# Performance work log

Measured on AMD Instinct MI355X. Metric: run time of the kernel, lower is better.

Reference implementation:

```python
import jax, jax.numpy as jnp
import numpy as np

B = 1024       # repertoires (batch)
TCR = 100      # instances (TCRs) per repertoire
FEAT = 15      # feature_num (conv in_channels)
AA = 24        # aa_num (sequence length)
KS = [2, 3, 4, 5, 6, 7]
FN = [3, 3, 3, 2, 2, 1]
NINP = 14      # sum(FN)
EPS = 1e-5     # BatchNorm eps


def sparsemax(z):
    # z: (B, K); sparsemax along axis 1 (Martins & Astudillo 2016)
    K = z.shape[1]
    zs = -jnp.sort(-z, axis=1)               # descending sort
    cs = jnp.cumsum(zs, axis=1)
    k = jnp.arange(1, K + 1, dtype=z.dtype)
    support = 1.0 + k * zs > cs              # (B, K) bool
    ksel = jnp.sum(support, axis=1, keepdims=True).astype(jnp.int32)  # support size
    tau = (jnp.take_along_axis(cs, ksel - 1, axis=1) - 1.0) / ksel.astype(z.dtype)
    return jnp.maximum(z - tau, 0.0)


def setup_inputs() -> dict:
    key = jax.random.key(0)
    ks = jax.random.split(key, 12)
    inp = {"x": jax.random.normal(ks[0], (B, TCR, FEAT, AA), dtype=jnp.float32)}
    for i, (h, f) in enumerate(zip(KS, FN)):
        inp[f"cw{i}"] = jax.random.normal(ks[1 + i], (f, FEAT, h), dtype=jnp.float32) * 0.1
        inp[f"cb{i}"] = jnp.zeros((f,), dtype=jnp.float32)
    inp["fc1_w"] = jax.random.normal(ks[7], (NINP, NINP), dtype=jnp.float32) * 0.2
    inp["fc1_b"] = jnp.zeros((NINP,), dtype=jnp.float32)
    inp["waout_w"] = jax.random.normal(ks[8], (1, NINP), dtype=jnp.float32) * 0.2
    inp["decf_w"] = jax.random.normal(ks[9], (NINP, NINP), dtype=jnp.float32) * 0.2
    inp["decf_b"] = jnp.zeros((NINP,), dtype=jnp.float32)
    inp["bn_g"] = jnp.ones((NINP,), dtype=jnp.float32)
    inp["bn_b"] = jnp.zeros((NINP,), dtype=jnp.float32)
    inp["decs_w"] = jax.random.normal(ks[10], (2, NINP), dtype=jnp.float32) * 0.2
    inp["decs_b"] = jnp.zeros((2,), dtype=jnp.float32)
    return inp


def reference(x, cw0, cb0, cw1, cb1, cw2, cb2, cw3, cb3, cw4, cb4, cw5, cb5,
              fc1_w, fc1_b, waout_w, decf_w, decf_b, bn_g, bn_b, decs_w, decs_b):
    xf = x.reshape(-1, FEAT, AA)  # (B*TCR, 15, 24)
    feats = []
    for w, b in ((cw0, cb0), (cw1, cb1), (cw2, cb2), (cw3, cb3), (cw4, cb4), (cw5, cb5)):
        y = jax.lax.conv_general_dilated(xf, w, (1,), 'VALID',
                                         dimension_numbers=('NCH', 'OIH', 'NCH'))
        y = jax.nn.relu(y + b[None, :, None])
        feats.append(jnp.max(y, axis=-1))  # AdaptiveMaxPool1d(1): global max over length
    out = jnp.concatenate(feats, axis=1).reshape(-1, TCR, NINP)  # (B, TCR, 14)
    # fclayer1 + dropout(eval=identity) + relu; applied per-instance so the
    # torch (TCR, B, .) transpose is equivalent to working in (B, TCR, .)
    h = jax.nn.relu(out @ fc1_w.T + fc1_b)                       # (B, TCR, 14)
    attw = sparsemax(h @ waout_w[0])                             # (B, TCR)
    pooled = jnp.einsum('bt,btd->bd', attw, h)                   # bmm(attw[:,None,:], h)
    z = pooled @ decf_w.T + decf_b                               # decoder_f
    mu = jnp.mean(z, axis=0)                                     # BatchNorm1d (batch stats)
    var = jnp.var(z, axis=0)
    z = jax.nn.relu((z - mu) / jnp.sqrt(var + EPS) * bn_g + bn_b)
    logits = z @ decs_w.T + decs_b                               # decoder_s -> (B, 2)
    return logits, attw
```

## Files before the change

kernel.cpp:

```cpp
#include <hip/hip_runtime.h>

typedef unsigned int  u32;
typedef unsigned short u16;

__device__ __forceinline__ float bf2f(u16 u){
    return __uint_as_float(((u32)u) << 16);
}
__device__ __forceinline__ float lo16(u32 v){ return __uint_as_float(v << 16); }
__device__ __forceinline__ float hi16(u32 v){ return __uint_as_float(v & 0xffff0000u); }
__device__ __forceinline__ u16 f2bf(float f){
    u32 x = __float_as_uint(f);
    x += 0x7fffu + ((x >> 16) & 1u);
    return (u16)(x >> 16);
}
__device__ __forceinline__ float ldany(const void* p, int i, bool bf){
    return bf ? bf2f(((const u16*)p)[i]) : ((const float*)p)[i];
}

#define B_      1024
#define TCR_    100
#define NINST   (B_*TCR_)

#define OFF_WL     0
#define OFF_CB     840
#define OFF_FC1W   854
#define OFF_FC1B   1050
#define OFF_WA     1064
#define OFF_DECFW  1078
#define OFF_DECFB  1274
#define OFF_BNG    1288
#define OFF_BNB    1302
#define OFF_DECSW  1316
#define OFF_DECSB  1344

__global__ __launch_bounds__(256) void k_pack(
    const void* cw0, const void* cb0, const void* cw1, const void* cb1,
    const void* cw2, const void* cb2, const void* cw3, const void* cb3,
    const void* cw4, const void* cb4, const void* cw5, const void* cb5,
    const void* fc1_w, const void* fc1_b, const void* waout,
    const void* decf_w, const void* decf_b,
    const void* bn_g, const void* bn_b,
    const void* decs_w, const void* decs_b,
    float* __restrict__ wsP)
{
    const int tid = threadIdx.x;
    const bool bf = (((const u16*)bn_g)[0] == 0x3F80u);

    for (int widx = tid; widx < 840; widx += 256){
        float val;
        if (widx < 90)      { int e = widx;       int c=e/6,  rr=e-c*6,  ff=rr/2, j=rr-ff*2; val=ldany(cw0,(ff*15+c)*2+j,bf); }
        else if (widx < 225){ int e = widx - 90;  int c=e/9,  rr=e-c*9,  ff=rr/3, j=rr-ff*3; val=ldany(cw1,(ff*15+c)*3+j,bf); }
        else if (widx < 405){ int e = widx - 225; int c=e/12, rr=e-c*12, ff=rr/4, j=rr-ff*4; val=ldany(cw2,(ff*15+c)*4+j,bf); }
        else if (widx < 555){ int e = widx - 405; int c=e/10, rr=e-c*10, ff=rr/5, j=rr-ff*5; val=ldany(cw3,(ff*15+c)*5+j,bf); }
        else if (widx < 735){ int e = widx - 555; int c=e/12, rr=e-c*12, ff=rr/6, j=rr-ff*6; val=ldany(cw4,(ff*15+c)*6+j,bf); }
        else                { int e = widx - 735; int c=e/7,  j=e-c*7;                        val=ldany(cw5,c*7+j,bf); }
        wsP[OFF_WL + widx] = val;
    }
    for (int i = tid; i < 14; i += 256){
        float bv;
        if (i < 3)       bv = ldany(cb0, i, bf);
        else if (i < 6)  bv = ldany(cb1, i - 3, bf);
        else if (i < 9)  bv = ldany(cb2, i - 6, bf);
        else if (i < 11) bv = ldany(cb3, i - 9, bf);
        else if (i < 13) bv = ldany(cb4, i - 11, bf);
        else             bv = ldany(cb5, 0, bf);
        wsP[OFF_CB    + i] = bv;
        wsP[OFF_FC1B  + i] = ldany(fc1_b,  i, bf);
        wsP[OFF_WA    + i] = ldany(waout,  i, bf);
        wsP[OFF_DECFB + i] = ldany(decf_b, i, bf);
        wsP[OFF_BNG   + i] = ldany(bn_g,   i, bf);
        wsP[OFF_BNB   + i] = ldany(bn_b,   i, bf);
    }
    for (int i = tid; i < 196; i += 256){
        wsP[OFF_FC1W  + i] = ldany(fc1_w,  i, bf);
        wsP[OFF_DECFW + i] = ldany(decf_w, i, bf);
    }
    for (int i = tid; i < 28; i += 256) wsP[OFF_DECSW + i] = ldany(decs_w, i, bf);
    for (int i = tid; i < 2;  i += 256) wsP[OFF_DECSB + i] = ldany(decs_b, i, bf);
}

template<int H, int F, int WOFF>
__device__ __forceinline__ void acc_channel(float (&acc)[F][25 - H], const float* xr,
                                            const float* __restrict__ wsP, int c){
    float wv[F * H];
    const float* wc = wsP + WOFF + c * (F * H);
    #pragma unroll
    for (int k = 0; k < F * H; ++k) wv[k] = wc[k];
    #pragma unroll
    for (int ff = 0; ff < F; ++ff)
        #pragma unroll
        for (int t = 0; t < 25 - H; ++t)
            #pragma unroll
            for (int j = 0; j < H; ++j)
                acc[ff][t] = fmaf(wv[ff * H + j], xr[t + j], acc[ff][t]);
}

template<int H, int F, int OF>
__device__ __forceinline__ void group_max(float (&acc)[F][25 - H],
                                          const float* __restrict__ wsP, float* feats){
    #pragma unroll
    for (int ff = 0; ff < F; ++ff){
        float m = acc[ff][0];
        #pragma unroll
        for (int t = 1; t < 25 - H; ++t) m = fmaxf(m, acc[ff][t]);
        feats[OF + ff] = fmaxf(m + wsP[OFF_CB + OF + ff], 0.0f);
    }
}

template<bool BF>
__device__ __forceinline__ void unpackx(const uint4* buf, float* xr){
    constexpr int NB = BF ? 3 : 6;
    #pragma unroll
    for (int i = 0; i < NB; ++i){
        u32 w0 = buf[i].x, w1 = buf[i].y, w2 = buf[i].z, w3 = buf[i].w;
        if (BF){
            xr[i*8+0] = lo16(w0); xr[i*8+1] = hi16(w0);
            xr[i*8+2] = lo16(w1); xr[i*8+3] = hi16(w1);
            xr[i*8+4] = lo16(w2); xr[i*8+5] = hi16(w2);
            xr[i*8+6] = lo16(w3); xr[i*8+7] = hi16(w3);
        } else {
            xr[i*4+0] = __uint_as_float(w0); xr[i*4+1] = __uint_as_float(w1);
            xr[i*4+2] = __uint_as_float(w2); xr[i*4+3] = __uint_as_float(w3);
        }
    }
}

template<bool BF, int HA,int FA,int WA,int OFA, int HB,int FBn,int WB,int OFB>
__device__ __forceinline__ void conv_pass(const char* xb, const float* __restrict__ wsP,
                                          float* feats){
    constexpr int NB = BF ? 3 : 6;
    constexpr int CS = BF ? 48 : 96;
    float accA[FA][25 - HA];
    float accB[FBn][25 - HB];
    #pragma unroll
    for (int ff = 0; ff < FA; ++ff)
        #pragma unroll
        for (int t = 0; t < 25 - HA; ++t) accA[ff][t] = 0.0f;
    #pragma unroll
    for (int ff = 0; ff < FBn; ++ff)
        #pragma unroll
        for (int t = 0; t < 25 - HB; ++t) accB[ff][t] = 0.0f;

    uint4 buf[NB];
    {
        const uint4* p = (const uint4*)xb;
        #pragma unroll
        for (int i = 0; i < NB; ++i) buf[i] = p[i];
    }
    #pragma unroll 1
    for (int c = 0; c < 15; ++c){
        uint4 nbuf[NB];
        int cn = (c < 14) ? (c + 1) : 14;
        const uint4* pn = (const uint4*)(xb + cn * CS);
        #pragma unroll
        for (int i = 0; i < NB; ++i) nbuf[i] = pn[i];

        float xr[24];
        unpackx<BF>(buf, xr);
        acc_channel<HA, FA, WA>(accA, xr, wsP, c);
        acc_channel<HB, FBn, WB>(accB, xr, wsP, c);

        #pragma unroll
        for (int i = 0; i < NB; ++i) buf[i] = nbuf[i];
    }
    group_max<HA, FA, OFA>(accA, wsP, feats);
    group_max<HB, FBn, OFB>(accB, wsP, feats);
}

template<bool BF>
__device__ __forceinline__ void conv_body(const void* __restrict__ x,
                                          const float* __restrict__ wsP,
                                          float* __restrict__ hbufT,
                                          float* __restrict__ sbuf){
    const int inst = blockIdx.x * 64 + threadIdx.x;
    const char* xb = (const char*)x + (size_t)inst * (BF ? 720 : 1440);

    float feats[14];
    conv_pass<BF, 2,3,  0, 0,  7,1,735,13>(xb, wsP, feats);
    conv_pass<BF, 3,3, 90, 3,  6,2,555,11>(xb, wsP, feats);
    conv_pass<BF, 4,3,225, 6,  5,2,405, 9>(xb, wsP, feats);

    float hv[14];
    #pragma unroll
    for (int i = 0; i < 14; ++i){
        float a = wsP[OFF_FC1B + i];
        #pragma unroll
        for (int j = 0; j < 14; ++j) a = fmaf(feats[j], wsP[OFF_FC1W + i * 14 + j], a);
        hv[i] = fmaxf(a, 0.0f);
    }
    float sc = 0.0f;
    #pragma unroll
    for (int i = 0; i < 14; ++i) sc = fmaf(hv[i], wsP[OFF_WA + i], sc);

    #pragma unroll
    for (int d = 0; d < 14; ++d) hbufT[d * NINST + inst] = hv[d];
    sbuf[inst] = sc;
}

__global__ __launch_bounds__(64) void k_conv(
    const void* __restrict__ x, const float* __restrict__ wsP,
    const void* __restrict__ dt,
    float* __restrict__ hbufT, float* __restrict__ sbuf)
{
    const bool bf = (((const u16*)dt)[0] == 0x3F80u);
    if (bf) conv_body<true >(x, wsP, hbufT, sbuf);
    else    conv_body<false>(x, wsP, hbufT, sbuf);
}

__global__ __launch_bounds__(64) void k_sparse(
    const float* __restrict__ hbufT, const float* __restrict__ sbuf,
    const float* __restrict__ wsP, const void* __restrict__ dt,
    float* __restrict__ zbuf, void* __restrict__ d_out)
{
    const int b    = blockIdx.x;
    const int lane = threadIdx.x;
    const bool bf  = (((const u16*)dt)[0] == 0x3F80u);
    const bool has2 = lane < (TCR_ - 64);

    float z0 = sbuf[b * TCR_ + lane];
    float z1 = has2 ? sbuf[b * TCR_ + 64 + lane] : -1e30f;

    float m = fmaxf(z0, z1);
    #pragma unroll
    for (int o = 32; o; o >>= 1) m = fmaxf(m, __shfl_xor(m, o));

    float lo = m - 1.0f, hi = m;
    for (int it = 0; it < 32; ++it){
        float mid = 0.5f * (lo + hi);
        float s = fmaxf(z0 - mid, 0.0f) + fmaxf(z1 - mid, 0.0f);
        #pragma unroll
        for (int o = 32; o; o >>= 1) s += __shfl_xor(s, o);
        if (s >= 1.0f) lo = mid; else hi = mid;
    }
    float tau = 0.5f * (lo + hi);
    float a0 = fmaxf(z0 - tau, 0.0f);
    float a1 = fmaxf(z1 - tau, 0.0f);

    if (bf){
        u16* aw = (u16*)d_out + 2048;
        aw[b * TCR_ + lane] = f2bf(a0);
        if (has2) aw[b * TCR_ + 64 + lane] = f2bf(a1);
    } else {
        float* aw = (float*)d_out + 2048;
        aw[b * TCR_ + lane] = a0;
        if (has2) aw[b * TCR_ + 64 + lane] = a1;
    }

    float ap[14];
    #pragma unroll
    for (int d = 0; d < 14; ++d){
        float v = a0 * hbufT[d * NINST + b * TCR_ + lane];
        if (has2) v += a1 * hbufT[d * NINST + b * TCR_ + 64 + lane];
        #pragma unroll
        for (int o = 32; o; o >>= 1) v += __shfl_xor(v, o);
        ap[d] = v;
    }
    if (lane < 14){
        float zv = wsP[OFF_DECFB + lane];
        #pragma unroll
        for (int j = 0; j < 14; ++j) zv = fmaf(ap[j], wsP[OFF_DECFW + lane * 14 + j], zv);
        zbuf[b * 14 + lane] = zv;
    }
}

__global__ __launch_bounds__(256) void k_bn(
    const float* __restrict__ zbuf, const float* __restrict__ wsP,
    const void* __restrict__ dt, void* __restrict__ d_out)
{
    __shared__ float part[4][28];
    __shared__ float red[28];
    const int tid  = threadIdx.x;
    const int lane = tid & 63;
    const int w    = tid >> 6;
    const bool bf  = (((const u16*)dt)[0] == 0x3F80u);

    float z[4][14];
    #pragma unroll
    for (int r = 0; r < 4; ++r)
        #pragma unroll
        for (int d = 0; d < 14; ++d) z[r][d] = zbuf[(tid + 256 * r) * 14 + d];

    #pragma unroll
    for (int d = 0; d < 14; ++d){
        float s = 0.0f, q = 0.0f;
        #pragma unroll
        for (int r = 0; r < 4; ++r){ s += z[r][d]; q += z[r][d] * z[r][d]; }
        #pragma unroll
        for (int o = 32; o; o >>= 1){ s += __shfl_xor(s, o); q += __shfl_xor(q, o); }
        if (lane == 0){ part[w][d] = s; part[w][14 + d] = q; }
    }
    __syncthreads();
    if (tid < 28) red[tid] = part[0][tid] + part[1][tid] + part[2][tid] + part[3][tid];
    __syncthreads();

    float mu[14], rs[14];
    #pragma unroll
    for (int d = 0; d < 14; ++d){
        mu[d] = red[d] * (1.0f / 1024.0f);
        float var = red[14 + d] * (1.0f / 1024.0f) - mu[d] * mu[d];
        rs[d] = rsqrtf(var + 1e-5f);
    }
    #pragma unroll
    for (int r = 0; r < 4; ++r){
        float zn[14];
        #pragma unroll
        for (int d = 0; d < 14; ++d)
            zn[d] = fmaxf((z[r][d] - mu[d]) * rs[d] * wsP[OFF_BNG + d] + wsP[OFF_BNB + d], 0.0f);
        #pragma unroll
        for (int c = 0; c < 2; ++c){
            float a = wsP[OFF_DECSB + c];
            #pragma unroll
            for (int d = 0; d < 14; ++d) a = fmaf(zn[d], wsP[OFF_DECSW + c * 14 + d], a);
            if (bf) ((u16*)d_out)[(tid + 256 * r) * 2 + c] = f2bf(a);
            else    ((float*)d_out)[(tid + 256 * r) * 2 + c] = a;
        }
    }
}

extern "C" void kernel_launch(void* const* d_in, const int* in_sizes, int n_in,
                              void* d_out, int out_size, void* d_ws, size_t ws_size,
                              hipStream_t stream)
{
    (void)in_sizes; (void)n_in; (void)out_size; (void)ws_size;
    const void* x     = d_in[0];
    const void* bn_g  = d_in[18];

    float* wsP   = (float*)d_ws;
    float* hbufT = wsP + 2048;
    float* sbuf  = hbufT + (size_t)14 * NINST;
    float* zbuf  = sbuf + NINST;

    k_pack<<<1, 256, 0, stream>>>(
        d_in[1], d_in[2], d_in[3], d_in[4], d_in[5], d_in[6],
        d_in[7], d_in[8], d_in[9], d_in[10], d_in[11], d_in[12],
        d_in[13], d_in[14], d_in[15], d_in[16], d_in[17],
        d_in[18], d_in[19], d_in[20], d_in[21], wsP);
    k_conv<<<NINST / 64, 64, 0, stream>>>(x, wsP, bn_g, hbufT, sbuf);
    k_sparse<<<B_, 64, 0, stream>>>(hbufT, sbuf, wsP, bn_g, zbuf, d_out);
    k_bn<<<1, 256, 0, stream>>>(zbuf, wsP, bn_g, d_out);
}
```

Baseline: 359.3 us.

## Split each instance across two threads and fuse all conv filters into one pass

Each TCR instance is now handled by a pair of threads. Each thread loads an overlapping 16-position window of the sequence, and the pair combines partial maxima with a lane shuffle. The three separate passes over the 15 channels are merged into a single pass that accumulates all six filter widths. This needs a repacked per-channel weight layout of 56 floats per channel. The aim is to read x once instead of three times and to double the thread-level parallelism, in exchange for some redundant overlap computation and a larger live accumulator set (about 180 floats per thread), which raises register pressure.

```diff
diff --git a/kernel.cpp b/kernel.cpp
--- a/kernel.cpp
+++ b/kernel.cpp
@@ -21,7 +21,7 @@
 #define TCR_    100
 #define NINST   (B_*TCR_)
 
-#define OFF_WL     0
+#define OFF_WCH    0
 #define OFF_CB     840
 #define OFF_FC1W   854
 #define OFF_FC1B   1050
@@ -47,14 +47,14 @@
     const bool bf = (((const u16*)bn_g)[0] == 0x3F80u);
 
     for (int widx = tid; widx < 840; widx += 256){
-        float val;
-        if (widx < 90)      { int e = widx;       int c=e/6,  rr=e-c*6,  ff=rr/2, j=rr-ff*2; val=ldany(cw0,(ff*15+c)*2+j,bf); }
-        else if (widx < 225){ int e = widx - 90;  int c=e/9,  rr=e-c*9,  ff=rr/3, j=rr-ff*3; val=ldany(cw1,(ff*15+c)*3+j,bf); }
-        else if (widx < 405){ int e = widx - 225; int c=e/12, rr=e-c*12, ff=rr/4, j=rr-ff*4; val=ldany(cw2,(ff*15+c)*4+j,bf); }
-        else if (widx < 555){ int e = widx - 405; int c=e/10, rr=e-c*10, ff=rr/5, j=rr-ff*5; val=ldany(cw3,(ff*15+c)*5+j,bf); }
-        else if (widx < 735){ int e = widx - 555; int c=e/12, rr=e-c*12, ff=rr/6, j=rr-ff*6; val=ldany(cw4,(ff*15+c)*6+j,bf); }
-        else                { int e = widx - 735; int c=e/7,  j=e-c*7;                        val=ldany(cw5,c*7+j,bf); }
-        wsP[OFF_WL + widx] = val;
+        float val; int dst;
+        if (widx < 90)      { int e = widx;       int c=e/6,  rr=e-c*6,  ff=rr/2, j=rr-ff*2; val=ldany(cw0,(ff*15+c)*2+j,bf); dst=c*56+ 0+ff*2+j; }
+        else if (widx < 225){ int e = widx - 90;  int c=e/9,  rr=e-c*9,  ff=rr/3, j=rr-ff*3; val=ldany(cw1,(ff*15+c)*3+j,bf); dst=c*56+ 6+ff*3+j; }
+        else if (widx < 405){ int e = widx - 225; int c=e/12, rr=e-c*12, ff=rr/4, j=rr-ff*4; val=ldany(cw2,(ff*15+c)*4+j,bf); dst=c*56+15+ff*4+j; }
+        else if (widx < 555){ int e = widx - 405; int c=e/10, rr=e-c*10, ff=rr/5, j=rr-ff*5; val=ldany(cw3,(ff*15+c)*5+j,bf); dst=c*56+27+ff*5+j; }
+        else if (widx < 735){ int e = widx - 555; int c=e/12, rr=e-c*12, ff=rr/6, j=rr-ff*6; val=ldany(cw4,(ff*15+c)*6+j,bf); dst=c*56+37+ff*6+j; }
+        else                { int e = widx - 735; int c=e/7,  j=e-c*7;                        val=ldany(cw5,c*7+j,bf);        dst=c*56+49+j; }
+        wsP[OFF_WCH + dst] = val;
     }
     for (int i = tid; i < 14; i += 256){
         float bv;
@@ -79,92 +79,54 @@
     for (int i = tid; i < 2;  i += 256) wsP[OFF_DECSB + i] = ldany(decs_b, i, bf);
 }
 
-template<int H, int F, int WOFF>
-__device__ __forceinline__ void acc_channel(float (&acc)[F][25 - H], const float* xr,
-                                            const float* __restrict__ wsP, int c){
+template<int H, int F, int GOFF>
+__device__ __forceinline__ void acc_ch(float (&acc)[F][17 - H], const float* xr,
+                                       const float* __restrict__ wch){
     float wv[F * H];
-    const float* wc = wsP + WOFF + c * (F * H);
-    #pragma unroll
-    for (int k = 0; k < F * H; ++k) wv[k] = wc[k];
+    #pragma unroll
+    for (int k = 0; k < F * H; ++k) wv[k] = wch[GOFF + k];
     #pragma unroll
     for (int ff = 0; ff < F; ++ff)
         #pragma unroll
-        for (int t = 0; t < 25 - H; ++t)
+        for (int i = 0; i < 17 - H; ++i)
             #pragma unroll
             for (int j = 0; j < H; ++j)
-                acc[ff][t] = fmaf(wv[ff * H + j], xr[t + j], acc[ff][t]);
+                acc[ff][i] = fmaf(wv[ff * H + j], xr[i + j], acc[ff][i]);
 }
 
 template<int H, int F, int OF>
-__device__ __forceinline__ void group_max(float (&acc)[F][25 - H],
-                                          const float* __restrict__ wsP, float* feats){
+__device__ __forceinline__ void pair_max(float (&acc)[F][17 - H],
+                                         const float* __restrict__ wsP, float* feats){
     #pragma unroll
     for (int ff = 0; ff < F; ++ff){
         float m = acc[ff][0];
         #pragma unroll
-        for (int t = 1; t < 25 - H; ++t) m = fmaxf(m, acc[ff][t]);
+        for (int i = 1; i < 17 - H; ++i) m = fmaxf(m, acc[ff][i]);
+        m = fmaxf(m, __shfl_xor(m, 1));
         feats[OF + ff] = fmaxf(m + wsP[OFF_CB + OF + ff], 0.0f);
     }
 }
 
 template<bool BF>
-__device__ __forceinline__ void unpackx(const uint4* buf, float* xr){
-    constexpr int NB = BF ? 3 : 6;
-    #pragma unroll
-    for (int i = 0; i < NB; ++i){
-        u32 w0 = buf[i].x, w1 = buf[i].y, w2 = buf[i].z, w3 = buf[i].w;
-        if (BF){
+__device__ __forceinline__ void unpack16(const uint4* buf, float* xr){
+    if (BF){
+        #pragma unroll
+        for (int i = 0; i < 2; ++i){
+            u32 w0 = buf[i].x, w1 = buf[i].y, w2 = buf[i].z, w3 = buf[i].w;
             xr[i*8+0] = lo16(w0); xr[i*8+1] = hi16(w0);
             xr[i*8+2] = lo16(w1); xr[i*8+3] = hi16(w1);
             xr[i*8+4] = lo16(w2); xr[i*8+5] = hi16(w2);
             xr[i*8+6] = lo16(w3); xr[i*8+7] = hi16(w3);
-        } else {
-            xr[i*4+0] = __uint_as_float(w0); xr[i*4+1] = __uint_as_float(w1);
-            xr[i*4+2] = __uint_as_float(w2); xr[i*4+3] = __uint_as_float(w3);
         }
-    }
-}
-
-template<bool BF, int HA,int FA,int WA,int OFA, int HB,int FBn,int WB,int OFB>
-__device__ __forceinline__ void conv_pass(const char* xb, const float* __restrict__ wsP,
-                                          float* feats){
-    constexpr int NB = BF ? 3 : 6;
-    constexpr int CS = BF ? 48 : 96;
-    float accA[FA][25 - HA];
-    float accB[FBn][25 - HB];
-    #pragma unroll
-    for (int ff = 0; ff < FA; ++ff)
-        #pragma unroll
-        for (int t = 0; t < 25 - HA; ++t) accA[ff][t] = 0.0f;
-    #pragma unroll
-    for (int ff = 0; ff < FBn; ++ff)
-        #pragma unroll
-        for (int t = 0; t < 25 - HB; ++t) accB[ff][t] = 0.0f;
-
-    uint4 buf[NB];
-    {
-        const uint4* p = (const uint4*)xb;
-        #pragma unroll
-        for (int i = 0; i < NB; ++i) buf[i] = p[i];
-    }
-    #pragma unroll 1
-    for (int c = 0; c < 15; ++c){
-        uint4 nbuf[NB];
-        int cn = (c < 14) ? (c + 1) : 14;
-        const uint4* pn = (const uint4*)(xb + cn * CS);
-        #pragma unroll
-        for (int i = 0; i < NB; ++i) nbuf[i] = pn[i];
-
-        float xr[24];
-        unpackx<BF>(buf, xr);
-        acc_channel<HA, FA, WA>(accA, xr, wsP, c);
-        acc_channel<HB, FBn, WB>(accB, xr, wsP, c);
-
-        #pragma unroll
-        for (int i = 0; i < NB; ++i) buf[i] = nbuf[i];
-    }
-    group_max<HA, FA, OFA>(accA, wsP, feats);
-    group_max<HB, FBn, OFB>(accB, wsP, feats);
+    } else {
+        #pragma unroll
+        for (int i = 0; i < 4; ++i){
+            xr[i*4+0] = __uint_as_float(buf[i].x);
+            xr[i*4+1] = __uint_as_float(buf[i].y);
+            xr[i*4+2] = __uint_as_float(buf[i].z);
+            xr[i*4+3] = __uint_as_float(buf[i].w);
+        }
+    }
 }
 
 template<bool BF>
@@ -172,13 +134,69 @@
                                           const float* __restrict__ wsP,
                                           float* __restrict__ hbufT,
                                           float* __restrict__ sbuf){
-    const int inst = blockIdx.x * 64 + threadIdx.x;
-    const char* xb = (const char*)x + (size_t)inst * (BF ? 720 : 1440);
+    constexpr int NB = BF ? 2 : 4;
+    constexpr int CS = BF ? 48 : 96;
+    const int tid   = threadIdx.x;
+    const int tpart = tid & 1;
+    const int inst  = blockIdx.x * 128 + (tid >> 1);
+    const char* xb  = (const char*)x + (size_t)inst * (BF ? 720 : 1440)
+                                     + tpart * (BF ? 16 : 32);
+
+    float a2[3][15], a3[3][14], a4[3][13], a5[2][12], a6[2][11], a7[1][10];
+    #pragma unroll
+    for (int f = 0; f < 3; ++f){
+        #pragma unroll
+        for (int i = 0; i < 15; ++i) a2[f][i] = 0.0f;
+        #pragma unroll
+        for (int i = 0; i < 14; ++i) a3[f][i] = 0.0f;
+        #pragma unroll
+        for (int i = 0; i < 13; ++i) a4[f][i] = 0.0f;
+    }
+    #pragma unroll
+    for (int f = 0; f < 2; ++f){
+        #pragma unroll
+        for (int i = 0; i < 12; ++i) a5[f][i] = 0.0f;
+        #pragma unroll
+        for (int i = 0; i < 11; ++i) a6[f][i] = 0.0f;
+    }
+    #pragma unroll
+    for (int i = 0; i < 10; ++i) a7[0][i] = 0.0f;
+
+    uint4 cur[NB];
+    {
+        const uint4* p = (const uint4*)xb;
+        #pragma unroll
+        for (int i = 0; i < NB; ++i) cur[i] = p[i];
+    }
+    #pragma unroll 1
+    for (int c = 0; c < 15; ++c){
+        uint4 nxt[NB];
+        int cn = (c < 14) ? (c + 1) : 14;
+        const uint4* pn = (const uint4*)(xb + cn * CS);
+        #pragma unroll
+        for (int i = 0; i < NB; ++i) nxt[i] = pn[i];
+
+        float xr[16];
+        unpack16<BF>(cur, xr);
+        const float* wch = wsP + OFF_WCH + c * 56;
+        acc_ch<2,3, 0>(a2, xr, wch);
+        acc_ch<3,3, 6>(a3, xr, wch);
+        acc_ch<4,3,15>(a4, xr, wch);
+        acc_ch<5,2,27>(a5, xr, wch);
+        acc_ch<6,2,37>(a6, xr, wch);
+        acc_ch<7,1,49>(a7, xr, wch);
+
+        #pragma unroll
+        for (int i = 0; i < NB; ++i) cur[i] = nxt[i];
+    }
 
     float feats[14];
-    conv_pass<BF, 2,3,  0, 0,  7,1,735,13>(xb, wsP, feats);
-    conv_pass<BF, 3,3, 90, 3,  6,2,555,11>(xb, wsP, feats);
-    conv_pass<BF, 4,3,225, 6,  5,2,405, 9>(xb, wsP, feats);
+    pair_max<2,3, 0>(a2, wsP, feats);
+    pair_max<3,3, 3>(a3, wsP, feats);
+    pair_max<4,3, 6>(a4, wsP, feats);
+    pair_max<5,2, 9>(a5, wsP, feats);
+    pair_max<6,2,11>(a6, wsP, feats);
+    pair_max<7,1,13>(a7, wsP, feats);
 
     float hv[14];
     #pragma unroll
@@ -192,12 +210,14 @@
     #pragma unroll
     for (int i = 0; i < 14; ++i) sc = fmaf(hv[i], wsP[OFF_WA + i], sc);
 
-    #pragma unroll
-    for (int d = 0; d < 14; ++d) hbufT[d * NINST + inst] = hv[d];
-    sbuf[inst] = sc;
-}
-
-__global__ __launch_bounds__(64) void k_conv(
+    if (tpart == 0){
+        #pragma unroll
+        for (int d = 0; d < 14; ++d) hbufT[d * NINST + inst] = hv[d];
+        sbuf[inst] = sc;
+    }
+}
+
+__global__ __launch_bounds__(256) void k_conv(
     const void* __restrict__ x, const float* __restrict__ wsP,
     const void* __restrict__ dt,
     float* __restrict__ hbufT, float* __restrict__ sbuf)
@@ -335,7 +355,7 @@
         d_in[7], d_in[8], d_in[9], d_in[10], d_in[11], d_in[12],
         d_in[13], d_in[14], d_in[15], d_in[16], d_in[17],
         d_in[18], d_in[19], d_in[20], d_in[21], wsP);
-    k_conv<<<NINST / 64, 64, 0, stream>>>(x, wsP, bn_g, hbufT, sbuf);
+    k_conv<<<NINST / 128, 256, 0, stream>>>(x, wsP, bn_g, hbufT, sbuf);
     k_sparse<<<B_, 64, 0, stream>>>(hbufT, sbuf, wsP, bn_g, zbuf, d_out);
     k_bn<<<1, 256, 0, stream>>>(zbuf, wsP, bn_g, d_out);
 }
```

After: 298.3 us. 17.0% less time.
